# Kernel tuning notes

Measured on AMD Instinct MI355X. Metric: run time of the kernel, lower is better.

Reference implementation:

```python
import jax, jax.numpy as jnp
import numpy as np

B, N, CS = 4, 384, 384
CZ = 128
H, C, PQ, PV = 12, 16, 4, 8
INF, EPS = 1e5, 1e-8


def _rigid_apply(rot, trans, pts):
    # rot: [B,N,3,3], trans: [B,N,3], pts: [B,N,P,3]
    return jnp.einsum('bnij,bnpj->bnpi', rot, pts) + trans[:, :, None, :]


def _pts_from_linear(x, n_pts):
    # torch: split last dim into 3 chunks (x,y,z blocks) then stack on dim -1
    Bx, Nx = x.shape[:2]
    return jnp.moveaxis(x.reshape(Bx, Nx, 3, n_pts), -2, -1)  # [B,N,n_pts,3]


def _forward(s, z, rot, trans, mask, w_q, b_q, w_kv, b_kv, w_gq, b_gq, w_gk, b_gk,
             w_qp, b_qp, w_kvp, b_kvp, head_weights, w_out, b_out):
    del z  # z is an unused arg in the original forward
    Bx, Nx, _ = s.shape
    q = (s @ w_q + b_q).reshape(Bx, Nx, H, C)
    kv = (s @ w_kv + b_kv).reshape(Bx, Nx, H, 2 * C)
    k, v = kv[..., :C], kv[..., C:]
    # g_q / g_k are computed in the original but never used (dead code):
    _ = (s.sum(0) @ w_gq + b_gq)
    _ = (s.sum(0) @ w_gk + b_gk)

    q_pts = _pts_from_linear(s @ w_qp + b_qp, H * PQ)
    q_pts = _rigid_apply(rot, trans, q_pts).reshape(Bx, Nx, H, PQ, 3)
    kv_pts = _pts_from_linear(s @ w_kvp + b_kvp, H * (PQ + PV))
    kv_pts = _rigid_apply(rot, trans, kv_pts).reshape(Bx, Nx, H, PQ + PV, 3)
    k_pts, v_pts = kv_pts[..., :PQ, :], kv_pts[..., PQ:, :]

    scale = np.sqrt(1.0 / (3 * C)).astype(np.float32)
    a = jnp.einsum('bihc,bjhc->bhij', q, k) * scale  # [B,H,N,N]
    a_g = a  # original recomputes the identical q@k product

    # point-distance attention bias; diff is [B,N,N,H,PQ,3]
    diff = q_pts[:, :, None] - k_pts[:, None]
    sq = jnp.sum(diff * diff, axis=-1)  # [B,N,N,H,PQ]
    hw = jax.nn.softplus(head_weights) * np.sqrt(1.0 / (3 * (PQ * 9.0 / 2))).astype(np.float32)
    pt_att = -0.5 * jnp.sum(sq * hw[:, None], axis=-1)  # [B,N,N,H]
    pt_att = jnp.moveaxis(pt_att, -1, 1)  # [B,H,N,N]

    square_mask = INF * (mask[:, :, None] * mask[:, None, :] - 1.0)  # [B,N,N]
    a = jax.nn.softmax(a + square_mask[:, None] + a_g + pt_att, axis=-1)

    o = jnp.einsum('bhij,bjhc->bihc', a, v).reshape(Bx, Nx, H * C)
    o_pt = jnp.einsum('bhij,bjhpx->bihpx', a, v_pts)  # [B,N,H,PV,3]
    # invert_apply: rot^T (x - t)
    o_pt = jnp.einsum('bnji,bnhpj->bnhpi', rot, o_pt - trans[:, :, None, None, :])
    o_pt_norm = jnp.sqrt(jnp.sum(o_pt ** 2, axis=-1) + EPS).reshape(Bx, Nx, H * PV)
    o_pt = o_pt.reshape(Bx, Nx, H * PV, 3)
    cat = jnp.concatenate([o, o_pt[..., 0], o_pt[..., 1], o_pt[..., 2], o_pt_norm], axis=-1)
    return cat @ w_out + b_out


def setup_inputs() -> dict:
    key = jax.random.key(0)
    ks = jax.random.split(key, 16)
    lin = lambda k, fi, fo: jax.random.normal(k, (fi, fo), jnp.float32) / np.sqrt(fi).astype(np.float32)
    hc = H * C
    out_dim = H * (C + PV * 4)
    return {
        's': jax.random.normal(ks[0], (B, N, CS), jnp.float32),
        'z': jax.random.normal(ks[1], (B, N, N, CZ), jnp.float32),
        'rot': jnp.linalg.qr(jax.random.normal(ks[2], (B, N, 3, 3), jnp.float32))[0],
        'trans': jax.random.normal(ks[3], (B, N, 3), jnp.float32),
        'mask': jnp.ones((B, N), jnp.float32),
        'w_q': lin(ks[4], CS, hc), 'b_q': jnp.zeros((hc,), jnp.float32),
        'w_kv': lin(ks[5], CS, 2 * hc), 'b_kv': jnp.zeros((2 * hc,), jnp.float32),
        'w_gq': lin(ks[6], CS, hc), 'b_gq': jnp.zeros((hc,), jnp.float32),
        'w_gk': lin(ks[7], CS, hc), 'b_gk': jnp.zeros((hc,), jnp.float32),
        'w_qp': lin(ks[8], CS, H * PQ * 3), 'b_qp': jnp.zeros((H * PQ * 3,), jnp.float32),
        'w_kvp': lin(ks[9], CS, H * (PQ + PV) * 3), 'b_kvp': jnp.zeros((H * (PQ + PV) * 3,), jnp.float32),
        'head_weights': jnp.full((H,), 0.541324854, jnp.float32),  # softplus^-1(1)
        'w_out': lin(ks[10], out_dim, CS), 'b_out': jnp.zeros((CS,), jnp.float32),
    }


def reference(s, z, rot, trans, mask, w_q, b_q, w_kv, b_kv, w_gq, b_gq, w_gk, b_gk,
              w_qp, b_qp, w_kvp, b_kvp, head_weights, w_out, b_out):
    return _forward(s, z, rot, trans, mask, w_q, b_q, w_kv, b_kv, w_gq, b_gq, w_gk, b_gk,
                    w_qp, b_qp, w_kvp, b_kvp, head_weights, w_out, b_out)
```

## Files before the change

### kernel.cpp

```cpp
#include <hip/hip_runtime.h>
#include <math.h>

#define Bb 4
#define Nn 384
#define CSs 384
#define Hh 12
#define Cc 16
#define PQq 4
#define PVv 8
#define FPROJ 1152
#define FCAT 576
#define INFV 100000.0f
#define EPSV 1e-8f

#define WS_PROJ 0
#define WS_CAT  3022848
#define WS_PART 4423680
#define PSTRIDE 1408
#define WS_WT   9068544
#define WS_WTO  9289728
#define WS_AH   9400320
#define WS_AL   9695232
#define WS_KH   9990144
#define WS_KL   10285056
#define WS_VBP  10579968
#define WS_SB   10948608

typedef __attribute__((ext_vector_type(8))) short short8v;
typedef __attribute__((ext_vector_type(4))) float f32x4;

__device__ __forceinline__ short f2bf(float x) {
    unsigned u = __float_as_uint(x);
    unsigned r = (u + 0x7FFFu + ((u >> 16) & 1u)) >> 16;
    return (short)r;
}
__device__ __forceinline__ float bf2f(short h) {
    return __uint_as_float(((unsigned)(unsigned short)h) << 16);
}

__device__ __forceinline__ float get_bias(int f,
    const float* __restrict__ b_q, const float* __restrict__ b_kv,
    const float* __restrict__ b_qp, const float* __restrict__ b_kvp)
{
    if (f < 192) return b_q[f];
    if (f < 576) return b_kv[f - 192];
    if (f < 720) return b_qp[f - 576];
    return b_kvp[f - 720];
}

__global__ __launch_bounds__(256) void prep_kernel(
    const float* __restrict__ w_q, const float* __restrict__ w_kv,
    const float* __restrict__ w_qp, const float* __restrict__ w_kvp,
    const float* __restrict__ w_out, const float* __restrict__ s,
    short* __restrict__ wt, short* __restrict__ wto, short* __restrict__ sb)
{
    int idx = blockIdx.x * 256 + threadIdx.x;
    if (idx < 1152 * 384) {
        int f = idx / 384, k = idx % 384;
        float v;
        if (f < 192)      v = w_q[(size_t)k * 192 + f];
        else if (f < 576) v = w_kv[(size_t)k * 384 + (f - 192)];
        else if (f < 720) v = w_qp[(size_t)k * 144 + (f - 576)];
        else              v = w_kvp[(size_t)k * 432 + (f - 720)];
        wt[idx] = f2bf(v);
    } else if (idx < 1152 * 384 + 384 * 576) {
        int j = idx - 1152 * 384;
        int f = j / 576, k = j % 576;
        wto[j] = f2bf(w_out[(size_t)k * 384 + f]);
    } else if (idx < 1152 * 384 + 384 * 576 + 1536 * 384) {
        int j = idx - (1152 * 384 + 384 * 576);
        sb[j] = f2bf(s[j]);
    }
}

__global__ __launch_bounds__(256) void proj_kernel(
    const short* __restrict__ sb, const short* __restrict__ wt,
    const float* __restrict__ b_q, const float* __restrict__ b_kv,
    const float* __restrict__ b_qp, const float* __restrict__ b_kvp,
    float* __restrict__ proj)
{
    __shared__ short Al[64 * 40];
    __shared__ short Bl[64 * 40];

    const int bm = blockIdx.x % 24;
    const int bn = blockIdx.x / 24;
    const int m0 = bm * 64;
    const int f0 = bn * 64;
    const int t = threadIdx.x;
    const int w = t >> 6;
    const int lane = t & 63;
    const int lrow = lane & 15;
    const int lkg  = lane >> 4;

    const int srow = t >> 2;
    const int sseg = t & 3;

    f32x4 acc0 = {0,0,0,0}, acc1 = {0,0,0,0}, acc2 = {0,0,0,0}, acc3 = {0,0,0,0};

    for (int ks = 0; ks < 12; ++ks) {
        const int kbase = ks * 32;
        *(short8v*)&Al[srow * 40 + sseg * 8] =
            *(const short8v*)&sb[(size_t)(m0 + srow) * CSs + kbase + sseg * 8];
        *(short8v*)&Bl[srow * 40 + sseg * 8] =
            *(const short8v*)&wt[(size_t)(f0 + srow) * 384 + kbase + sseg * 8];
        __syncthreads();

        short8v av = *(const short8v*)&Al[(16 * w + lrow) * 40 + lkg * 8];
        short8v b0 = *(const short8v*)&Bl[(lrow) * 40 + lkg * 8];
        short8v b1 = *(const short8v*)&Bl[(16 + lrow) * 40 + lkg * 8];
        short8v b2 = *(const short8v*)&Bl[(32 + lrow) * 40 + lkg * 8];
        short8v b3 = *(const short8v*)&Bl[(48 + lrow) * 40 + lkg * 8];
        acc0 = __builtin_amdgcn_mfma_f32_16x16x32_bf16(av, b0, acc0, 0, 0, 0);
        acc1 = __builtin_amdgcn_mfma_f32_16x16x32_bf16(av, b1, acc1, 0, 0, 0);
        acc2 = __builtin_amdgcn_mfma_f32_16x16x32_bf16(av, b2, acc2, 0, 0, 0);
        acc3 = __builtin_amdgcn_mfma_f32_16x16x32_bf16(av, b3, acc3, 0, 0, 0);
        __syncthreads();
    }

    const int orow = m0 + 16 * w + lkg * 4;
#pragma unroll
    for (int e = 0; e < 4; ++e) {
        float* pr = proj + (size_t)(orow + e) * FPROJ + f0;
        int c0 = lrow;
        pr[c0]      = acc0[e] + get_bias(f0 + c0,      b_q, b_kv, b_qp, b_kvp);
        pr[16 + c0] = acc1[e] + get_bias(f0 + 16 + c0, b_q, b_kv, b_qp, b_kvp);
        pr[32 + c0] = acc2[e] + get_bias(f0 + 32 + c0, b_q, b_kv, b_qp, b_kvp);
        pr[48 + c0] = acc3[e] + get_bias(f0 + 48 + c0, b_q, b_kv, b_qp, b_kvp);
    }
}

__global__ __launch_bounds__(192) void pack_kernel(
    const float* __restrict__ proj,
    const float* __restrict__ rot, const float* __restrict__ trans,
    const float* __restrict__ hwts, const float* __restrict__ mask,
    short* __restrict__ Ah, short* __restrict__ Al,
    short* __restrict__ Kh, short* __restrict__ Kl,
    short* __restrict__ Vbp)
{
    __shared__ float abuf[12 * 32];
    __shared__ float kbuf[12 * 32];
    __shared__ float vbuf[12 * 40];
    __shared__ float kpsq[12 * 4];

    const int bn = blockIdx.x;
    const int b = bn / Nn;
    const int n = bn % Nn;
    const int t = threadIdx.x;
    const float* R = rot + (size_t)bn * 9;
    const float* T = trans + (size_t)bn * 3;
    const float* pr = proj + (size_t)bn * FPROJ;
    const float mi = mask[bn];

    if (t < 144) {
        float x = pr[720 + t];
        float y = pr[720 + 144 + t];
        float z = pr[720 + 288 + t];
        float ox = R[0]*x + R[1]*y + R[2]*z + T[0];
        float oy = R[3]*x + R[4]*y + R[5]*z + T[1];
        float oz = R[6]*x + R[7]*y + R[8]*z + T[2];
        int h = t / 12, pp = t % 12;
        if (pp < PQq) {
            kbuf[h*32 + 16 + pp*3 + 0] = ox;
            kbuf[h*32 + 16 + pp*3 + 1] = oy;
            kbuf[h*32 + 16 + pp*3 + 2] = oz;
            kpsq[h*4 + pp] = ox*ox + oy*oy + oz*oz;
        } else {
            vbuf[h*40 + 16 + (pp - PQq)*3 + 0] = ox;
            vbuf[h*40 + 16 + (pp - PQq)*3 + 1] = oy;
            vbuf[h*40 + 16 + (pp - PQq)*3 + 2] = oz;
        }
    }
    if (t < 48) {
        float x = pr[576 + t];
        float y = pr[576 + 48 + t];
        float z = pr[576 + 96 + t];
        float ox = R[0]*x + R[1]*y + R[2]*z + T[0];
        float oy = R[3]*x + R[4]*y + R[5]*z + T[1];
        float oz = R[6]*x + R[7]*y + R[8]*z + T[2];
        int h = t / 4, p = t % 4;
        float n2wc = log1pf(expf(hwts[h])) * 0.13608276348795434f;
        abuf[h*32 + 16 + p*3 + 0] = n2wc * ox;
        abuf[h*32 + 16 + p*3 + 1] = n2wc * oy;
        abuf[h*32 + 16 + p*3 + 2] = n2wc * oz;
    }
    {
        int h = t >> 4, c = t & 15;
        abuf[h*32 + c] = 0.28867513459481287f * pr[h * 16 + c];
        kbuf[h*32 + c] = pr[192 + h * 32 + c];
        vbuf[h*40 + c] = pr[192 + h * 32 + 16 + c];
    }
    if (t < 12) {
        abuf[t*32 + 28] = 1.0f;  abuf[t*32 + 29] = mi;
        abuf[t*32 + 30] = 0.0f;  abuf[t*32 + 31] = 0.0f;
        kbuf[t*32 + 29] = INFV * (mi - 1.0f);
        kbuf[t*32 + 30] = 0.0f;  kbuf[t*32 + 31] = 0.0f;
    }
    __syncthreads();
    if (t < 12) {
        float hw2 = log1pf(expf(hwts[t]));
        float wc = -0.5f * hw2 * 0.13608276348795434f;
        kbuf[t*32 + 28] = wc * (kpsq[t*4] + kpsq[t*4+1] + kpsq[t*4+2] + kpsq[t*4+3]);
    }
    __syncthreads();

    if (t < 48) {
        int h = t >> 2, pc = t & 3;
        const float* src = &abuf[h*32 + pc*8];
        short8v hi, lo;
#pragma unroll
        for (int k = 0; k < 8; ++k) {
            short hh = f2bf(src[k]);
            hi[k] = hh; lo[k] = f2bf(src[k] - bf2f(hh));
        }
        size_t off = ((size_t)((b * Hh + h) * Nn + n)) * 32 + pc * 8;
        *(short8v*)&Ah[off] = hi;
        *(short8v*)&Al[off] = lo;
    } else if (t < 96) {
        int tt = t - 48, h = tt >> 2, pc = tt & 3;
        const float* src = &kbuf[h*32 + pc*8];
        short8v hi, lo;
#pragma unroll
        for (int k = 0; k < 8; ++k) {
            short hh = f2bf(src[k]);
            hi[k] = hh; lo[k] = f2bf(src[k] - bf2f(hh));
        }
        size_t off = ((size_t)((b * Hh + h) * Nn + n)) * 32 + pc * 8;
        *(short8v*)&Kh[off] = hi;
        *(short8v*)&Kl[off] = lo;
    } else if (t < 156) {
        int tt = t - 96, h = tt / 5, pc = tt % 5;
        const float* src = &vbuf[h*40 + pc*8];
        short8v v;
#pragma unroll
        for (int k = 0; k < 8; ++k) v[k] = f2bf(src[k]);
        *(short8v*)&Vbp[((size_t)((b * Hh + h) * Nn + n)) * 40 + pc * 8] = v;
    }
}

__global__ __launch_bounds__(256) void attn_part_kernel(
    const short* __restrict__ Ah, const short* __restrict__ Al,
    const short* __restrict__ Kh, const short* __restrict__ Kl,
    const short* __restrict__ Vbp,
    float* __restrict__ part)
{
    __shared__ short smem_s[13696];
    short* Ahi = smem_s;
    short* Alo = smem_s + 2560;
    short* Khi = smem_s + 5120;
    short* Klo = smem_s + 7680;
    short* Vb  = smem_s + 10240;
    short* Pb  = smem_s;

    const int bid = blockIdx.x;
    const int jc = bid % 6;
    const int ic = (bid / 6) % 6;
    const int h  = (bid / 36) % Hh;
    const int b  = bid / (36 * Hh);
    const int t  = threadIdx.x;
    const int i0 = ic * 64;
    const int j0 = jc * 64;
    const int bh = b * Hh + h;

    const short* AhB = Ah + ((size_t)(bh * Nn + i0)) * 32;
    const short* AlB = Al + ((size_t)(bh * Nn + i0)) * 32;
    const short* KhB = Kh + ((size_t)(bh * Nn + j0)) * 32;
    const short* KlB = Kl + ((size_t)(bh * Nn + j0)) * 32;
    const short* VbB = Vbp + ((size_t)(bh * Nn + j0)) * 40;

    {
        const int i = t >> 2, pc = t & 3;
        *(short8v*)&Ahi[i * 40 + pc * 8] = *(const short8v*)&AhB[i * 32 + pc * 8];
        *(short8v*)&Alo[i * 40 + pc * 8] = *(const short8v*)&AlB[i * 32 + pc * 8];
        *(short8v*)&Khi[i * 40 + pc * 8] = *(const short8v*)&KhB[i * 32 + pc * 8];
        *(short8v*)&Klo[i * 40 + pc * 8] = *(const short8v*)&KlB[i * 32 + pc * 8];
    }
#pragma unroll
    for (int e = t; e < 320; e += 256) {
        int j = e / 5, pc = e % 5;
        short8v v = *(const short8v*)&VbB[j * 40 + pc * 8];
#pragma unroll
        for (int k = 0; k < 8; ++k) Vb[(pc * 8 + k) * 72 + j] = v[k];
    }
    if (t < 144) {
        int o = 40 * 72 + t * 4;
        Vb[o] = 0; Vb[o+1] = 0; Vb[o+2] = 0; Vb[o+3] = 0;
    }
    __syncthreads();

    const int w = t >> 6;
    const int lane = t & 63;
    const int lrow = lane & 15;
    const int lkg  = lane >> 4;

    f32x4 La0 = {0,0,0,0}, La1 = {0,0,0,0}, La2 = {0,0,0,0}, La3 = {0,0,0,0};
    {
        short8v ahi = *(const short8v*)&Ahi[(16 * w + lrow) * 40 + lkg * 8];
        short8v alo = *(const short8v*)&Alo[(16 * w + lrow) * 40 + lkg * 8];
        short8v k0h = *(const short8v*)&Khi[(lrow) * 40 + lkg * 8];
        short8v k1h = *(const short8v*)&Khi[(16 + lrow) * 40 + lkg * 8];
        short8v k2h = *(const short8v*)&Khi[(32 + lrow) * 40 + lkg * 8];
        short8v k3h = *(const short8v*)&Khi[(48 + lrow) * 40 + lkg * 8];
        short8v k0l = *(const short8v*)&Klo[(lrow) * 40 + lkg * 8];
        short8v k1l = *(const short8v*)&Klo[(16 + lrow) * 40 + lkg * 8];
        short8v k2l = *(const short8v*)&Klo[(32 + lrow) * 40 + lkg * 8];
        short8v k3l = *(const short8v*)&Klo[(48 + lrow) * 40 + lkg * 8];
        La0 = __builtin_amdgcn_mfma_f32_16x16x32_bf16(ahi, k0h, La0, 0, 0, 0);
        La1 = __builtin_amdgcn_mfma_f32_16x16x32_bf16(ahi, k1h, La1, 0, 0, 0);
        La2 = __builtin_amdgcn_mfma_f32_16x16x32_bf16(ahi, k2h, La2, 0, 0, 0);
        La3 = __builtin_amdgcn_mfma_f32_16x16x32_bf16(ahi, k3h, La3, 0, 0, 0);
        La0 = __builtin_amdgcn_mfma_f32_16x16x32_bf16(alo, k0h, La0, 0, 0, 0);
        La1 = __builtin_amdgcn_mfma_f32_16x16x32_bf16(alo, k1h, La1, 0, 0, 0);
        La2 = __builtin_amdgcn_mfma_f32_16x16x32_bf16(alo, k2h, La2, 0, 0, 0);
        La3 = __builtin_amdgcn_mfma_f32_16x16x32_bf16(alo, k3h, La3, 0, 0, 0);
        La0 = __builtin_amdgcn_mfma_f32_16x16x32_bf16(ahi, k0l, La0, 0, 0, 0);
        La1 = __builtin_amdgcn_mfma_f32_16x16x32_bf16(ahi, k1l, La1, 0, 0, 0);
        La2 = __builtin_amdgcn_mfma_f32_16x16x32_bf16(ahi, k2l, La2, 0, 0, 0);
        La3 = __builtin_amdgcn_mfma_f32_16x16x32_bf16(ahi, k3l, La3, 0, 0, 0);
    }

    const size_t pidx = ((size_t)(bh * 6 + ic)) * 6 + jc;
    float* po = part + pidx * PSTRIDE;
    short* poO = (short*)po;

    float m0_, m1_, m2_, m3_, s0_, s1_, s2_, s3_;
    float p00,p10,p20,p30, p01,p11,p21,p31, p02,p12,p22,p32, p03,p13,p23,p33;

#define SMAX_E(E, TM, SM, P0, P1, P2, P3) { \
    float tmax_ = fmaxf(fmaxf(La0[E], La1[E]), fmaxf(La2[E], La3[E])); \
    tmax_ = fmaxf(tmax_, __shfl_xor(tmax_, 1)); \
    tmax_ = fmaxf(tmax_, __shfl_xor(tmax_, 2)); \
    tmax_ = fmaxf(tmax_, __shfl_xor(tmax_, 4)); \
    tmax_ = fmaxf(tmax_, __shfl_xor(tmax_, 8)); \
    P0 = __expf(La0[E] - tmax_); P1 = __expf(La1[E] - tmax_); \
    P2 = __expf(La2[E] - tmax_); P3 = __expf(La3[E] - tmax_); \
    float cs_ = P0 + P1 + P2 + P3; \
    cs_ += __shfl_xor(cs_, 1); cs_ += __shfl_xor(cs_, 2); \
    cs_ += __shfl_xor(cs_, 4); cs_ += __shfl_xor(cs_, 8); \
    TM = tmax_; SM = cs_; }

    SMAX_E(0, m0_, s0_, p00, p10, p20, p30);
    SMAX_E(1, m1_, s1_, p01, p11, p21, p31);
    SMAX_E(2, m2_, s2_, p02, p12, p22, p32);
    SMAX_E(3, m3_, s3_, p03, p13, p23, p33);
#undef SMAX_E

    if (lrow == 0) {
        int rb = 16 * w + 4 * lkg;
        po[1280 + rb + 0] = m0_; po[1344 + rb + 0] = s0_;
        po[1280 + rb + 1] = m1_; po[1344 + rb + 1] = s1_;
        po[1280 + rb + 2] = m2_; po[1344 + rb + 2] = s2_;
        po[1280 + rb + 3] = m3_; po[1344 + rb + 3] = s3_;
    }
    __syncthreads();

#define PW(E, PJ0, PJ1, PJ2, PJ3) { \
    int r_ = (16 * w + 4 * lkg + E) * 72; \
    Pb[r_ + lrow]      = f2bf(PJ0); \
    Pb[r_ + 16 + lrow] = f2bf(PJ1); \
    Pb[r_ + 32 + lrow] = f2bf(PJ2); \
    Pb[r_ + 48 + lrow] = f2bf(PJ3); }
    PW(0, p00, p10, p20, p30);
    PW(1, p01, p11, p21, p31);
    PW(2, p02, p12, p22, p32);
    PW(3, p03, p13, p23, p33);
#undef PW
    __syncthreads();

    f32x4 O0 = {0,0,0,0}, O1 = {0,0,0,0}, O2 = {0,0,0,0};
#pragma unroll
    for (int ch = 0; ch < 2; ++ch) {
        short8v pf = *(const short8v*)&Pb[(16 * w + lrow) * 72 + ch * 32 + lkg * 8];
        short8v v0 = *(const short8v*)&Vb[(lrow) * 72 + ch * 32 + lkg * 8];
        short8v v1 = *(const short8v*)&Vb[(16 + lrow) * 72 + ch * 32 + lkg * 8];
        short8v v2 = *(const short8v*)&Vb[(32 + lrow) * 72 + ch * 32 + lkg * 8];
        O0 = __builtin_amdgcn_mfma_f32_16x16x32_bf16(pf, v0, O0, 0, 0, 0);
        O1 = __builtin_amdgcn_mfma_f32_16x16x32_bf16(pf, v1, O1, 0, 0, 0);
        O2 = __builtin_amdgcn_mfma_f32_16x16x32_bf16(pf, v2, O2, 0, 0, 0);
    }
#pragma unroll
    for (int e = 0; e < 4; ++e) {
        int r = 16 * w + 4 * lkg + e;
        poO[r * 40 + lrow]      = f2bf(O0[e]);
        poO[r * 40 + 16 + lrow] = f2bf(O1[e]);
        if (lrow < 8) poO[r * 40 + 32 + lrow] = f2bf(O2[e]);
    }
}

__global__ __launch_bounds__(256) void attn_merge_kernel(
    const float* __restrict__ part,
    const float* __restrict__ rot, const float* __restrict__ trans,
    short* __restrict__ cat_bf)
{
    __shared__ float wsh[64 * 8];
    __shared__ float ob[64 * 44];

    const int bid = blockIdx.x;
    const int ic = bid % 6;
    const int h  = (bid / 6) % Hh;
    const int b  = bid / (6 * Hh);
    const int t  = threadIdx.x;
    const int i0 = ic * 64;
    const int bh = b * Hh + h;
    const size_t pbase = (((size_t)(bh * 6 + ic)) * 6) * PSTRIDE;

    if (t < 64) {
        float mk[6], sk[6];
        float M = -3.0e38f;
#pragma unroll
        for (int k = 0; k < 6; ++k) {
            mk[k] = part[pbase + (size_t)k * PSTRIDE + 1280 + t];
            sk[k] = part[pbase + (size_t)k * PSTRIDE + 1344 + t];
            M = fmaxf(M, mk[k]);
        }
        float wk[6]; float stot = 0.0f;
#pragma unroll
        for (int k = 0; k < 6; ++k) {
            wk[k] = __expf(mk[k] - M);
            stot += wk[k] * sk[k];
        }
        float inv = 1.0f / stot;
#pragma unroll
        for (int k = 0; k < 6; ++k) wsh[t * 8 + k] = wk[k] * inv;
    }
    __syncthreads();

#pragma unroll
    for (int it = 0; it < 10; ++it) {
        int idx = t + it * 256;
        int row = idx / 40, col = idx % 40;
        float v = 0.0f;
#pragma unroll
        for (int k = 0; k < 6; ++k) {
            const short* pO = (const short*)&part[pbase + (size_t)k * PSTRIDE];
            v += wsh[row * 8 + k] * bf2f(pO[row * 40 + col]);
        }
        ob[row * 44 + col] = v;
    }
    __syncthreads();

    {
        const int i = t >> 2;
        const int qq = t & 3;
        const int bnI = b * Nn + i0 + i;
        short* crow = cat_bf + (size_t)bnI * FCAT;

        float4 o = *(const float4*)&ob[i * 44 + 4 * qq];
        crow[h * 16 + 4 * qq + 0] = f2bf(o.x);
        crow[h * 16 + 4 * qq + 1] = f2bf(o.y);
        crow[h * 16 + 4 * qq + 2] = f2bf(o.z);
        crow[h * 16 + 4 * qq + 3] = f2bf(o.w);

        const float* R = rot + (size_t)bnI * 9;
        const float* T = trans + (size_t)bnI * 3;
#pragma unroll
        for (int e = 0; e < 2; ++e) {
            int pe = qq + 4 * e;
            float g0 = ob[i * 44 + 16 + 3 * pe + 0] - T[0];
            float g1 = ob[i * 44 + 16 + 3 * pe + 1] - T[1];
            float g2 = ob[i * 44 + 16 + 3 * pe + 2] - T[2];
            float lx = R[0]*g0 + R[3]*g1 + R[6]*g2;
            float ly = R[1]*g0 + R[4]*g1 + R[7]*g2;
            float lz = R[2]*g0 + R[5]*g1 + R[8]*g2;
            crow[192 + h * 8 + pe] = f2bf(lx);
            crow[288 + h * 8 + pe] = f2bf(ly);
            crow[384 + h * 8 + pe] = f2bf(lz);
            crow[480 + h * 8 + pe] = f2bf(sqrtf(lx*lx + ly*ly + lz*lz + EPSV));
        }
    }
}

__global__ __launch_bounds__(256) void out_kernel(
    const short* __restrict__ cat_bf, const short* __restrict__ wto,
    const float* __restrict__ b_out, float* __restrict__ out)
{
    __shared__ short Al[32 * 40];
    __shared__ short Bl[64 * 40];

    const int bm = blockIdx.x % 48;
    const int bn = blockIdx.x / 48;
    const int m0 = bm * 32;
    const int n0 = bn * 64;
    const int t = threadIdx.x;
    const int w = t >> 6;
    const int lane = t & 63;
    const int lrow = lane & 15;
    const int lkg  = lane >> 4;
    const int r0 = 16 * (w & 1);
    const int c0 = 32 * (w >> 1);

    f32x4 acc0 = {0,0,0,0}, acc1 = {0,0,0,0};

    for (int ks = 0; ks < 18; ++ks) {
        const int kbase = ks * 32;
        if (t < 128) {
            int arow = t >> 2, aseg = t & 3;
            *(short8v*)&Al[arow * 40 + aseg * 8] =
                *(const short8v*)&cat_bf[(size_t)(m0 + arow) * FCAT + kbase + aseg * 8];
        }
        {
            int brow = t >> 2, bseg = t & 3;
            *(short8v*)&Bl[brow * 40 + bseg * 8] =
                *(const short8v*)&wto[(size_t)(n0 + brow) * FCAT + kbase + bseg * 8];
        }
        __syncthreads();

        short8v av = *(const short8v*)&Al[(r0 + lrow) * 40 + lkg * 8];
        short8v b0 = *(const short8v*)&Bl[(c0 + lrow) * 40 + lkg * 8];
        short8v b1 = *(const short8v*)&Bl[(c0 + 16 + lrow) * 40 + lkg * 8];
        acc0 = __builtin_amdgcn_mfma_f32_16x16x32_bf16(av, b0, acc0, 0, 0, 0);
        acc1 = __builtin_amdgcn_mfma_f32_16x16x32_bf16(av, b1, acc1, 0, 0, 0);
        __syncthreads();
    }

    const int orow = m0 + r0 + lkg * 4;
#pragma unroll
    for (int e = 0; e < 4; ++e) {
        float* pr = out + (size_t)(orow + e) * 384 + n0 + c0;
        pr[lrow]      = acc0[e] + b_out[n0 + c0 + lrow];
        pr[16 + lrow] = acc1[e] + b_out[n0 + c0 + 16 + lrow];
    }
}

extern "C" void kernel_launch(void* const* d_in, const int* in_sizes, int n_in,
                              void* d_out, int out_size, void* d_ws, size_t ws_size,
                              hipStream_t stream) {
    const float* s     = (const float*)d_in[0];
    const float* rot   = (const float*)d_in[2];
    const float* trans = (const float*)d_in[3];
    const float* mask  = (const float*)d_in[4];
    const float* w_q   = (const float*)d_in[5];
    const float* b_q   = (const float*)d_in[6];
    const float* w_kv  = (const float*)d_in[7];
    const float* b_kv  = (const float*)d_in[8];
    const float* w_qp  = (const float*)d_in[13];
    const float* b_qp  = (const float*)d_in[14];
    const float* w_kvp = (const float*)d_in[15];
    const float* b_kvp = (const float*)d_in[16];
    const float* hwts  = (const float*)d_in[17];
    const float* w_out = (const float*)d_in[18];
    const float* b_out = (const float*)d_in[19];

    float* ws     = (float*)d_ws;
    float* proj   = ws + WS_PROJ;
    short* cat_bf = (short*)(ws + WS_CAT);
    float* partb  = ws + WS_PART;
    short* wt     = (short*)(ws + WS_WT);
    short* wto    = (short*)(ws + WS_WTO);
    short* Ah     = (short*)(ws + WS_AH);
    short* Alp    = (short*)(ws + WS_AL);
    short* Kh     = (short*)(ws + WS_KH);
    short* Kl     = (short*)(ws + WS_KL);
    short* Vbp    = (short*)(ws + WS_VBP);
    short* sb     = (short*)(ws + WS_SB);
    float* out    = (float*)d_out;

    hipLaunchKernelGGL(prep_kernel, dim3(4896), dim3(256), 0, stream,
                       w_q, w_kv, w_qp, w_kvp, w_out, s, wt, wto, sb);
    hipLaunchKernelGGL(proj_kernel, dim3(432), dim3(256), 0, stream,
                       sb, wt, b_q, b_kv, b_qp, b_kvp, proj);
    hipLaunchKernelGGL(pack_kernel, dim3(1536), dim3(192), 0, stream,
                       proj, rot, trans, hwts, mask, Ah, Alp, Kh, Kl, Vbp);
    hipLaunchKernelGGL(attn_part_kernel, dim3(1728), dim3(256), 0, stream,
                       Ah, Alp, Kh, Kl, Vbp, partb);
    hipLaunchKernelGGL(attn_merge_kernel, dim3(288), dim3(256), 0, stream,
                       partb, rot, trans, cat_bf);
    hipLaunchKernelGGL(out_kernel, dim3(288), dim3(256), 0, stream,
                       cat_bf, wto, b_out, out);
}
```

Measured before the change: 54.21 us.

## Fold bf16 conversion into GEMM loads and merge attention via last-block counter

Drops the separate prep kernel: the projection and output GEMMs now read fp32 s and weights directly and convert to bf16 while staging tiles in shared memory. Weight tiles are read with strided column loads instead of from a pre-transposed copy. The attention merge kernel is folded into the partial-attention kernel: an atomic counter per (b,h,i-chunk) picks the last finishing block, which then performs the merge. This removes two launches and an intermediate buffer round trip. In exchange it adds a memset, less coalesced weight loads, repeated conversion work across blocks, and a serialized merge tail inside the attention kernel.

```diff
diff --git a/kernel.cpp b/kernel.cpp
--- a/kernel.cpp
+++ b/kernel.cpp
@@ -17,14 +17,12 @@
 #define WS_CAT  3022848
 #define WS_PART 4423680
 #define PSTRIDE 1408
-#define WS_WT   9068544
-#define WS_WTO  9289728
+#define WS_CNT  9068544
 #define WS_AH   9400320
 #define WS_AL   9695232
 #define WS_KH   9990144
 #define WS_KL   10285056
 #define WS_VBP  10579968
-#define WS_SB   10948608
 
 typedef __attribute__((ext_vector_type(8))) short short8v;
 typedef __attribute__((ext_vector_type(4))) float f32x4;
@@ -48,33 +46,10 @@
     return b_kvp[f - 720];
 }
 
-__global__ __launch_bounds__(256) void prep_kernel(
+__global__ __launch_bounds__(256) void proj_kernel(
+    const float* __restrict__ s,
     const float* __restrict__ w_q, const float* __restrict__ w_kv,
     const float* __restrict__ w_qp, const float* __restrict__ w_kvp,
-    const float* __restrict__ w_out, const float* __restrict__ s,
-    short* __restrict__ wt, short* __restrict__ wto, short* __restrict__ sb)
-{
-    int idx = blockIdx.x * 256 + threadIdx.x;
-    if (idx < 1152 * 384) {
-        int f = idx / 384, k = idx % 384;
-        float v;
-        if (f < 192)      v = w_q[(size_t)k * 192 + f];
-        else if (f < 576) v = w_kv[(size_t)k * 384 + (f - 192)];
-        else if (f < 720) v = w_qp[(size_t)k * 144 + (f - 576)];
-        else              v = w_kvp[(size_t)k * 432 + (f - 720)];
-        wt[idx] = f2bf(v);
-    } else if (idx < 1152 * 384 + 384 * 576) {
-        int j = idx - 1152 * 384;
-        int f = j / 576, k = j % 576;
-        wto[j] = f2bf(w_out[(size_t)k * 384 + f]);
-    } else if (idx < 1152 * 384 + 384 * 576 + 1536 * 384) {
-        int j = idx - (1152 * 384 + 384 * 576);
-        sb[j] = f2bf(s[j]);
-    }
-}
-
-__global__ __launch_bounds__(256) void proj_kernel(
-    const short* __restrict__ sb, const short* __restrict__ wt,
     const float* __restrict__ b_q, const float* __restrict__ b_kv,
     const float* __restrict__ b_qp, const float* __restrict__ b_kvp,
     float* __restrict__ proj)
@@ -94,15 +69,38 @@
 
     const int srow = t >> 2;
     const int sseg = t & 3;
+    const int fl   = t & 63;
+    const int kk8  = t >> 6;
+
+    const float* wsrc; int ldw; int colof;
+    {
+        int f = f0 + fl;
+        if (f < 192)      { wsrc = w_q;   ldw = 192; colof = f; }
+        else if (f < 576) { wsrc = w_kv;  ldw = 384; colof = f - 192; }
+        else if (f < 720) { wsrc = w_qp;  ldw = 144; colof = f - 576; }
+        else              { wsrc = w_kvp; ldw = 432; colof = f - 720; }
+    }
 
     f32x4 acc0 = {0,0,0,0}, acc1 = {0,0,0,0}, acc2 = {0,0,0,0}, acc3 = {0,0,0,0};
 
     for (int ks = 0; ks < 12; ++ks) {
         const int kbase = ks * 32;
-        *(short8v*)&Al[srow * 40 + sseg * 8] =
-            *(const short8v*)&sb[(size_t)(m0 + srow) * CSs + kbase + sseg * 8];
-        *(short8v*)&Bl[srow * 40 + sseg * 8] =
-            *(const short8v*)&wt[(size_t)(f0 + srow) * 384 + kbase + sseg * 8];
+        {
+            const float* sp = s + (size_t)(m0 + srow) * CSs + kbase + sseg * 8;
+            float4 v0 = *(const float4*)sp;
+            float4 v1 = *(const float4*)(sp + 4);
+            short8v a;
+            a[0]=f2bf(v0.x); a[1]=f2bf(v0.y); a[2]=f2bf(v0.z); a[3]=f2bf(v0.w);
+            a[4]=f2bf(v1.x); a[5]=f2bf(v1.y); a[6]=f2bf(v1.z); a[7]=f2bf(v1.w);
+            *(short8v*)&Al[srow * 40 + sseg * 8] = a;
+        }
+        {
+            const float* wp = wsrc + (size_t)(kbase + kk8 * 8) * ldw + colof;
+            short8v bv;
+#pragma unroll
+            for (int j = 0; j < 8; ++j) bv[j] = f2bf(wp[(size_t)j * ldw]);
+            *(short8v*)&Bl[fl * 40 + kk8 * 8] = bv;
+        }
         __syncthreads();
 
         short8v av = *(const short8v*)&Al[(16 * w + lrow) * 40 + lkg * 8];
@@ -241,9 +239,12 @@
     const short* __restrict__ Ah, const short* __restrict__ Al,
     const short* __restrict__ Kh, const short* __restrict__ Kl,
     const short* __restrict__ Vbp,
-    float* __restrict__ part)
+    const float* __restrict__ rot, const float* __restrict__ trans,
+    float* __restrict__ part, int* __restrict__ cnt,
+    short* __restrict__ cat_bf)
 {
     __shared__ short smem_s[13696];
+    __shared__ int is_last;
     short* Ahi = smem_s;
     short* Alo = smem_s + 2560;
     short* Khi = smem_s + 5120;
@@ -260,6 +261,7 @@
     const int i0 = ic * 64;
     const int j0 = jc * 64;
     const int bh = b * Hh + h;
+    const int g  = bh * 6 + ic;
 
     const short* AhB = Ah + ((size_t)(bh * Nn + i0)) * 32;
     const short* AlB = Al + ((size_t)(bh * Nn + i0)) * 32;
@@ -318,8 +320,7 @@
         La3 = __builtin_amdgcn_mfma_f32_16x16x32_bf16(ahi, k3l, La3, 0, 0, 0);
     }
 
-    const size_t pidx = ((size_t)(bh * 6 + ic)) * 6 + jc;
-    float* po = part + pidx * PSTRIDE;
+    float* po = part + (size_t)(g * 6 + jc) * PSTRIDE;
     short* poO = (short*)po;
 
     float m0_, m1_, m2_, m3_, s0_, s1_, s2_, s3_;
@@ -384,24 +385,19 @@
         poO[r * 40 + 16 + lrow] = f2bf(O1[e]);
         if (lrow < 8) poO[r * 40 + 32 + lrow] = f2bf(O2[e]);
     }
-}
-
-__global__ __launch_bounds__(256) void attn_merge_kernel(
-    const float* __restrict__ part,
-    const float* __restrict__ rot, const float* __restrict__ trans,
-    short* __restrict__ cat_bf)
-{
-    __shared__ float wsh[64 * 8];
-    __shared__ float ob[64 * 44];
-
-    const int bid = blockIdx.x;
-    const int ic = bid % 6;
-    const int h  = (bid / 6) % Hh;
-    const int b  = bid / (6 * Hh);
-    const int t  = threadIdx.x;
-    const int i0 = ic * 64;
-    const int bh = b * Hh + h;
-    const size_t pbase = (((size_t)(bh * 6 + ic)) * 6) * PSTRIDE;
+
+    __syncthreads();
+    if (t == 0) {
+        __threadfence();
+        is_last = (atomicAdd(&cnt[g], 1) == 5);
+    }
+    __syncthreads();
+    if (!is_last) return;
+    __threadfence();
+
+    float* wsh = (float*)smem_s;
+    float* ob  = (float*)smem_s + 512;
+    const size_t pbase = (size_t)g * 6 * PSTRIDE;
 
     if (t < 64) {
         float mk[6], sk[6];
@@ -444,11 +440,14 @@
         const int bnI = b * Nn + i0 + i;
         short* crow = cat_bf + (size_t)bnI * FCAT;
 
-        float4 o = *(const float4*)&ob[i * 44 + 4 * qq];
-        crow[h * 16 + 4 * qq + 0] = f2bf(o.x);
-        crow[h * 16 + 4 * qq + 1] = f2bf(o.y);
-        crow[h * 16 + 4 * qq + 2] = f2bf(o.z);
-        crow[h * 16 + 4 * qq + 3] = f2bf(o.w);
+        float o0 = ob[i * 44 + 4 * qq + 0];
+        float o1 = ob[i * 44 + 4 * qq + 1];
+        float o2 = ob[i * 44 + 4 * qq + 2];
+        float o3 = ob[i * 44 + 4 * qq + 3];
+        crow[h * 16 + 4 * qq + 0] = f2bf(o0);
+        crow[h * 16 + 4 * qq + 1] = f2bf(o1);
+        crow[h * 16 + 4 * qq + 2] = f2bf(o2);
+        crow[h * 16 + 4 * qq + 3] = f2bf(o3);
 
         const float* R = rot + (size_t)bnI * 9;
         const float* T = trans + (size_t)bnI * 3;
@@ -470,7 +469,7 @@
 }
 
 __global__ __launch_bounds__(256) void out_kernel(
-    const short* __restrict__ cat_bf, const short* __restrict__ wto,
+    const short* __restrict__ cat_bf, const float* __restrict__ w_out,
     const float* __restrict__ b_out, float* __restrict__ out)
 {
     __shared__ short Al[32 * 40];
@@ -487,6 +486,8 @@
     const int lkg  = lane >> 4;
     const int r0 = 16 * (w & 1);
     const int c0 = 32 * (w >> 1);
+    const int nl  = t & 63;
+    const int kk8 = t >> 6;
 
     f32x4 acc0 = {0,0,0,0}, acc1 = {0,0,0,0};
 
@@ -498,9 +499,11 @@
                 *(const short8v*)&cat_bf[(size_t)(m0 + arow) * FCAT + kbase + aseg * 8];
         }
         {
-            int brow = t >> 2, bseg = t & 3;
-            *(short8v*)&Bl[brow * 40 + bseg * 8] =
-                *(const short8v*)&wto[(size_t)(n0 + brow) * FCAT + kbase + bseg * 8];
+            const float* wp = w_out + (size_t)(kbase + kk8 * 8) * 384 + n0 + nl;
+            short8v bv;
+#pragma unroll
+            for (int j = 0; j < 8; ++j) bv[j] = f2bf(wp[(size_t)j * 384]);
+            *(short8v*)&Bl[nl * 40 + kk8 * 8] = bv;
         }
         __syncthreads();
 
@@ -544,26 +547,21 @@
     float* proj   = ws + WS_PROJ;
     short* cat_bf = (short*)(ws + WS_CAT);
     float* partb  = ws + WS_PART;
-    short* wt     = (short*)(ws + WS_WT);
-    short* wto    = (short*)(ws + WS_WTO);
+    int*   cnt    = (int*)(ws + WS_CNT);
     short* Ah     = (short*)(ws + WS_AH);
     short* Alp    = (short*)(ws + WS_AL);
     short* Kh     = (short*)(ws + WS_KH);
     short* Kl     = (short*)(ws + WS_KL);
     short* Vbp    = (short*)(ws + WS_VBP);
-    short* sb     = (short*)(ws + WS_SB);
     float* out    = (float*)d_out;
 
-    hipLaunchKernelGGL(prep_kernel, dim3(4896), dim3(256), 0, stream,
-                       w_q, w_kv, w_qp, w_kvp, w_out, s, wt, wto, sb);
+    hipMemsetAsync(cnt, 0, 288 * sizeof(int), stream);
     hipLaunchKernelGGL(proj_kernel, dim3(432), dim3(256), 0, stream,
-                       sb, wt, b_q, b_kv, b_qp, b_kvp, proj);
+                       s, w_q, w_kv, w_qp, w_kvp, b_q, b_kv, b_qp, b_kvp, proj);
     hipLaunchKernelGGL(pack_kernel, dim3(1536), dim3(192), 0, stream,
                        proj, rot, trans, hwts, mask, Ah, Alp, Kh, Kl, Vbp);
     hipLaunchKernelGGL(attn_part_kernel, dim3(1728), dim3(256), 0, stream,
-                       Ah, Alp, Kh, Kl, Vbp, partb);
-    hipLaunchKernelGGL(attn_merge_kernel, dim3(288), dim3(256), 0, stream,
-                       partb, rot, trans, cat_bf);
+                       Ah, Alp, Kh, Kl, Vbp, rot, trans, partb, cnt, cat_bf);
     hipLaunchKernelGGL(out_kernel, dim3(288), dim3(256), 0, stream,
-                       cat_bf, wto, b_out, out);
-}
+                       cat_bf, w_out, b_out, out);
+}
```

Measured after the change: 208.7 us. 3.85x slower.
